# Performance work log

Hardware: AMD Instinct MI355X
Metric: run time of the kernel (lower is better)

The kernel has to match this reference:

```python
import jax, jax.numpy as jnp
import numpy as np

NEG = -9e15

def setup_inputs() -> dict:
    key = jax.random.key(0)
    k1, k2, k3, k4, k5, k6 = jax.random.split(key, 6)
    N, Fin, Fout = 8192, 256, 128
    inp = jax.random.normal(k1, (N, Fin), dtype=jnp.float32)
    adj = jax.random.randint(k2, (N, N), 0, 2, dtype=jnp.int32)
    W_w = jax.random.normal(k3, (Fout, Fin), dtype=jnp.float32) / np.sqrt(Fin)
    W_b = jax.random.normal(k4, (Fout,), dtype=jnp.float32) * 0.01
    a_w = jax.random.normal(k5, (1, 2 * Fout), dtype=jnp.float32) / np.sqrt(2 * Fout)
    a_b = jax.random.normal(k6, (1,), dtype=jnp.float32) * 0.01
    return {"input": inp, "adj": adj, "W_w": W_w, "W_b": W_b, "a_w": a_w, "a_b": a_b}

def reference(input, adj, W_w, W_b, a_w, a_b):
    alpha = 0.2
    Fout = W_w.shape[0]
    h = input @ W_w.T + W_b                      # [N, Fout]
    # a([h_i || h_j]) = a1.h_i + a2.h_j + b  (exact decomposition of concat+linear)
    a1 = a_w[0, :Fout]
    a2 = a_w[0, Fout:]
    e = jax.nn.leaky_relu((h @ a1)[:, None] + (h @ a2)[None, :] + a_b[0],
                          negative_slope=alpha)   # [N, N]
    scores = jnp.where(adj > 0, e, NEG)
    attention = jax.nn.softmax(scores, axis=1)    # dropout in eval mode = identity
    h_prime = attention @ h                       # [N, Fout]
    return jax.nn.elu(h_prime)
```

## Files before the change

kernel.cpp:

```cpp
#include <hip/hip_runtime.h>
#include <hip/hip_bf16.h>
#include <cmath>

#define NN 8192
#define FIN 256
#define FOUT 128
#define NCH 8
#define JC (NN / NCH)
#define WPC (JC / 64)
#define LOG2E 1.44269504f

typedef short short8 __attribute__((ext_vector_type(8)));
typedef float f32x4 __attribute__((ext_vector_type(4)));
typedef float f32x16 __attribute__((ext_vector_type(16)));
typedef unsigned long long u64;

static __device__ __forceinline__ unsigned short f2bf(float f) {
    unsigned u = __float_as_uint(f);
    u += 0x7fffu + ((u >> 16) & 1u);
    return (unsigned short)(u >> 16);
}

static __device__ __forceinline__ unsigned cvtpk(float lo, float hi) {
    unsigned r;
    asm("v_cvt_pk_bf16_f32 %0, %1, %2" : "=v"(r) : "v"(lo), "v"(hi));
    return r;
}

__global__ __launch_bounds__(256, 2)
void gat_stage(const float* __restrict__ input, const int* __restrict__ adj,
               const float* __restrict__ W, const float* __restrict__ Wb,
               const float* __restrict__ aw, const float* __restrict__ ab,
               unsigned short* __restrict__ hT4, float* __restrict__ s_out,
               float* __restrict__ t_out, u64* __restrict__ bm3) {
    __shared__ float sred[4][32];
    __shared__ float tred[4][32];
    const int tid = threadIdx.x;

    if (blockIdx.x >= 128) {
        const int row = (blockIdx.x - 128) * 2 + (tid >> 7);
        const int wing = tid & 127;
        const int4* p = (const int4*)(adj + (size_t)row * NN + wing * 64);
        u64 m = 0;
        #pragma unroll
        for (int q = 0; q < 16; ++q) {
            const int4 v = p[q];
            m |= (u64)(v.x > 0) << (q * 4 + 0);
            m |= (u64)(v.y > 0) << (q * 4 + 1);
            m |= (u64)(v.z > 0) << (q * 4 + 2);
            m |= (u64)(v.w > 0) << (q * 4 + 3);
        }
        const int ch = wing >> 4, winc = wing & 15;
        bm3[((size_t)ch * NN + row) * 16 + winc] = m;
        return;
    }

    const int w = tid >> 6, l = tid & 63;
    const int l5 = l >> 5, l31 = l & 31;
    const int nt = w >> 1, mh = w & 1;
    const int bx = blockIdx.x;
    const int i = bx * 64 + nt * 32 + l31;

    f32x16 acc0 = {}; f32x16 acc1 = {};
    #pragma unroll
    for (int ks = 0; ks < FIN / 16; ++ks) {
        const int c0 = ks * 16 + l5 * 8;
        const float4 b0 = *(const float4*)(input + (size_t)i * FIN + c0);
        const float4 b1 = *(const float4*)(input + (size_t)i * FIN + c0 + 4);
        short8 bf;
        bf[0]=(short)f2bf(b0.x); bf[1]=(short)f2bf(b0.y); bf[2]=(short)f2bf(b0.z); bf[3]=(short)f2bf(b0.w);
        bf[4]=(short)f2bf(b1.x); bf[5]=(short)f2bf(b1.y); bf[6]=(short)f2bf(b1.z); bf[7]=(short)f2bf(b1.w);
        {
            const int kcol = l31 + 32 * (2 * mh + 0);
            const float4 a0 = *(const float4*)(W + (size_t)kcol * FIN + c0);
            const float4 a1 = *(const float4*)(W + (size_t)kcol * FIN + c0 + 4);
            short8 af;
            af[0]=(short)f2bf(a0.x); af[1]=(short)f2bf(a0.y); af[2]=(short)f2bf(a0.z); af[3]=(short)f2bf(a0.w);
            af[4]=(short)f2bf(a1.x); af[5]=(short)f2bf(a1.y); af[6]=(short)f2bf(a1.z); af[7]=(short)f2bf(a1.w);
            acc0 = __builtin_amdgcn_mfma_f32_32x32x16_bf16(af, bf, acc0, 0, 0, 0);
        }
        {
            const int kcol = l31 + 32 * (2 * mh + 1);
            const float4 a0 = *(const float4*)(W + (size_t)kcol * FIN + c0);
            const float4 a1 = *(const float4*)(W + (size_t)kcol * FIN + c0 + 4);
            short8 af;
            af[0]=(short)f2bf(a0.x); af[1]=(short)f2bf(a0.y); af[2]=(short)f2bf(a0.z); af[3]=(short)f2bf(a0.w);
            af[4]=(short)f2bf(a1.x); af[5]=(short)f2bf(a1.y); af[6]=(short)f2bf(a1.z); af[7]=(short)f2bf(a1.w);
            acc1 = __builtin_amdgcn_mfma_f32_32x32x16_bf16(af, bf, acc1, 0, 0, 0);
        }
    }
    float sacc = 0.f, tacc = 0.f;
    const int jt = bx * 2 + nt;
    const int lane_half = 16 * (l31 >> 3);
    const int e4 = l31 & 7;
    #pragma unroll
    for (int m = 0; m < 2; ++m) {
        #pragma unroll
        for (int r = 0; r < 16; ++r) {
            const int kcol = 32 * (2 * mh + m) + 4 * l5 + (r & 3) + 8 * (r >> 2);
            const float hv = (m ? acc1[r] : acc0[r]) + Wb[kcol];
            const int lane4 = (kcol & 15) + lane_half;
            hT4[(size_t)(jt * 8 + (kcol >> 4)) * 512 + lane4 * 8 + e4] = f2bf(hv);
            sacc += hv * aw[kcol];
            tacc += hv * aw[FOUT + kcol];
        }
    }
    sacc += __shfl_xor(sacc, 32);
    tacc += __shfl_xor(tacc, 32);
    if (l < 32) { sred[w][l] = sacc; tred[w][l] = tacc; }
    __syncthreads();
    if (mh == 0 && l < 32) {
        s_out[i] = (sred[w][l] + sred[w + 1][l]) * LOG2E;
        t_out[i] = (tred[w][l] + tred[w + 1][l] + ab[0]) * LOG2E;
    }
}

__global__ __launch_bounds__(256, 4)
void gat_pass_b(const u64* __restrict__ bm3, const unsigned short* __restrict__ hT4,
                const float* __restrict__ s_in, const float* __restrict__ t_in,
                float* __restrict__ numw, float* __restrict__ dpart) {
    __shared__ int4 hbuf[2][1024];
    __shared__ float tlds[JC];
    const int tid = threadIdx.x;
    const int wv = tid >> 6, l = tid & 63;
    const int li = l & 15;
    const int kq = l >> 4;
    const int i0 = blockIdx.x * 64;
    const int chunk = blockIdx.y;
    const int jb = chunk * JC;

    *(float4*)&tlds[tid * 4] = *(const float4*)(t_in + jb + tid * 4);

    const int4* gsrc = (const int4*)hT4 + (size_t)chunk * 32 * 512;
    hbuf[0][tid]       = gsrc[tid];
    hbuf[0][tid + 256] = gsrc[tid + 256];
    hbuf[0][tid + 512] = gsrc[tid + 512];
    hbuf[0][tid + 768] = gsrc[tid + 768];

    const int lrow = wv * 16 + li;
    const float si = s_in[i0 + lrow];
    const u64* bmrow = bm3 + ((size_t)chunk * NN + i0 + lrow) * 16;
    u64 mcur = bmrow[0];
    __syncthreads();

    f32x4 acc0 = {}, acc1 = {}, acc2 = {}, acc3 = {};
    f32x4 acc4 = {}, acc5 = {}, acc6 = {}, acc7 = {};
    f32x4 accd = {};
    short8 ones;
    #pragma unroll
    for (int e = 0; e < 8; ++e) ones[e] = (short)0x3F80;

    for (int w = 0; w < WPC; ++w) {
        const int buf = w & 1;
        int4 g0, g1, g2, g3;
        u64 mnext = mcur;
        if (w + 1 < WPC) {
            const int4* gn = gsrc + (size_t)(w + 1) * 1024;
            g0 = gn[tid];
            g1 = gn[tid + 256];
            g2 = gn[tid + 512];
            g3 = gn[tid + 768];
            mnext = bmrow[w + 1];
        }
        #pragma unroll
        for (int kk = 0; kk < 2; ++kk) {
            const int4* hb = &hbuf[buf][kk * 512];
            const short8 af0 = *(const short8*)&hb[0 * 64 + l];
            const short8 af1 = *(const short8*)&hb[1 * 64 + l];
            const short8 af2 = *(const short8*)&hb[2 * 64 + l];
            const short8 af3 = *(const short8*)&hb[3 * 64 + l];
            const short8 af4 = *(const short8*)&hb[4 * 64 + l];
            const short8 af5 = *(const short8*)&hb[5 * 64 + l];
            const short8 af6 = *(const short8*)&hb[6 * 64 + l];
            const short8 af7 = *(const short8*)&hb[7 * 64 + l];
            const int tix = w * 64 + kk * 32 + kq * 8;
            const float4 t0 = *(const float4*)&tlds[tix];
            const float4 t1 = *(const float4*)&tlds[tix + 4];
            const unsigned mk = (unsigned)(mcur >> (kk * 32 + kq * 8)) & 0xffu;

            float x, p0, p1, p2, p3, p4, p5, p6, p7;
            x = si + t0.x; x = fmaxf(x, 0.2f * x); p0 = exp2f(x);
            p0 = (mk & 1u)   ? p0 : 0.f;
            x = si + t0.y; x = fmaxf(x, 0.2f * x); p1 = exp2f(x);
            p1 = (mk & 2u)   ? p1 : 0.f;
            x = si + t0.z; x = fmaxf(x, 0.2f * x); p2 = exp2f(x);
            p2 = (mk & 4u)   ? p2 : 0.f;
            x = si + t0.w; x = fmaxf(x, 0.2f * x); p3 = exp2f(x);
            p3 = (mk & 8u)   ? p3 : 0.f;
            x = si + t1.x; x = fmaxf(x, 0.2f * x); p4 = exp2f(x);
            p4 = (mk & 16u)  ? p4 : 0.f;
            x = si + t1.y; x = fmaxf(x, 0.2f * x); p5 = exp2f(x);
            p5 = (mk & 32u)  ? p5 : 0.f;
            x = si + t1.z; x = fmaxf(x, 0.2f * x); p6 = exp2f(x);
            p6 = (mk & 64u)  ? p6 : 0.f;
            x = si + t1.w; x = fmaxf(x, 0.2f * x); p7 = exp2f(x);
            p7 = (mk & 128u) ? p7 : 0.f;

            union { int4 i4; short8 s8; } bu;
            bu.i4.x = (int)cvtpk(p0, p1);
            bu.i4.y = (int)cvtpk(p2, p3);
            bu.i4.z = (int)cvtpk(p4, p5);
            bu.i4.w = (int)cvtpk(p6, p7);
            const short8 bf = bu.s8;

            acc0 = __builtin_amdgcn_mfma_f32_16x16x32_bf16(af0, bf, acc0, 0, 0, 0);
            acc1 = __builtin_amdgcn_mfma_f32_16x16x32_bf16(af1, bf, acc1, 0, 0, 0);
            acc2 = __builtin_amdgcn_mfma_f32_16x16x32_bf16(af2, bf, acc2, 0, 0, 0);
            acc3 = __builtin_amdgcn_mfma_f32_16x16x32_bf16(af3, bf, acc3, 0, 0, 0);
            acc4 = __builtin_amdgcn_mfma_f32_16x16x32_bf16(af4, bf, acc4, 0, 0, 0);
            acc5 = __builtin_amdgcn_mfma_f32_16x16x32_bf16(af5, bf, acc5, 0, 0, 0);
            acc6 = __builtin_amdgcn_mfma_f32_16x16x32_bf16(af6, bf, acc6, 0, 0, 0);
            acc7 = __builtin_amdgcn_mfma_f32_16x16x32_bf16(af7, bf, acc7, 0, 0, 0);
            accd = __builtin_amdgcn_mfma_f32_16x16x32_bf16(ones, bf, accd, 0, 0, 0);
        }
        if (w + 1 < WPC) {
            hbuf[buf ^ 1][tid]       = g0;
            hbuf[buf ^ 1][tid + 256] = g1;
            hbuf[buf ^ 1][tid + 512] = g2;
            hbuf[buf ^ 1][tid + 768] = g3;
        }
        mcur = mnext;
        __syncthreads();
    }

    float* nb = numw + (size_t)chunk * FOUT * NN;
    const int irow = i0 + lrow;
    #pragma unroll
    for (int r = 0; r < 4; ++r) {
        const int fr = kq * 4 + r;
        nb[(size_t)(fr      ) * NN + irow] = acc0[r];
        nb[(size_t)(fr + 16 ) * NN + irow] = acc1[r];
        nb[(size_t)(fr + 32 ) * NN + irow] = acc2[r];
        nb[(size_t)(fr + 48 ) * NN + irow] = acc3[r];
        nb[(size_t)(fr + 64 ) * NN + irow] = acc4[r];
        nb[(size_t)(fr + 80 ) * NN + irow] = acc5[r];
        nb[(size_t)(fr + 96 ) * NN + irow] = acc6[r];
        nb[(size_t)(fr + 112) * NN + irow] = acc7[r];
    }
    if (l < 16) dpart[(size_t)chunk * NN + i0 + wv * 16 + l] = accd[0];
}

__global__ __launch_bounds__(256)
void gat_reduce(const float* __restrict__ numw, const float* __restrict__ dpart,
                float* __restrict__ out, int nchunk) {
    __shared__ float tile[FOUT * 33];
    __shared__ float dent[32];
    const int t = threadIdx.x;
    const int i0 = blockIdx.x * 32;
    if (t < 32) {
        float d = 0.f;
        for (int c = 0; c < nchunk; ++c) d += dpart[(size_t)c * NN + i0 + t];
        dent[t] = d;
    }
    __syncthreads();
    #pragma unroll
    for (int e = 0; e < 4; ++e) {
        const int f = e * 32 + (t >> 3);
        const int io = (t & 7) * 4;
        float4 s = {0.f, 0.f, 0.f, 0.f};
        for (int c = 0; c < nchunk; ++c) {
            const float4 v = *(const float4*)(numw + ((size_t)c * FOUT + f) * NN + i0 + io);
            s.x += v.x; s.y += v.y; s.z += v.z; s.w += v.w;
        }
        float v;
        v = s.x / dent[io + 0]; tile[f * 33 + io + 0] = (v > 0.f) ? v : expm1f(v);
        v = s.y / dent[io + 1]; tile[f * 33 + io + 1] = (v > 0.f) ? v : expm1f(v);
        v = s.z / dent[io + 2]; tile[f * 33 + io + 2] = (v > 0.f) ? v : expm1f(v);
        v = s.w / dent[io + 3]; tile[f * 33 + io + 3] = (v > 0.f) ? v : expm1f(v);
    }
    __syncthreads();
    #pragma unroll
    for (int e = 0; e < 4; ++e) {
        const int row = (t >> 5) * 4 + e;
        const int fo = (t & 31) * 4;
        const float4 v = { tile[(fo + 0) * 33 + row], tile[(fo + 1) * 33 + row],
                           tile[(fo + 2) * 33 + row], tile[(fo + 3) * 33 + row] };
        *(float4*)(out + (size_t)(i0 + row) * FOUT + fo) = v;
    }
}

extern "C" void kernel_launch(void* const* d_in, const int* in_sizes, int n_in,
                              void* d_out, int out_size, void* d_ws, size_t ws_size,
                              hipStream_t stream) {
    const float* input = (const float*)d_in[0];
    const int*   adj   = (const int*)d_in[1];
    const float* Ww    = (const float*)d_in[2];
    const float* Wb    = (const float*)d_in[3];
    const float* aw    = (const float*)d_in[4];
    const float* ab    = (const float*)d_in[5];
    float* out = (float*)d_out;

    char* ws = (char*)d_ws;
    unsigned short* hT4 = (unsigned short*)ws;
    float* s_buf = (float*)(ws + (size_t)FOUT * NN * 2);
    float* t_buf = s_buf + NN;
    float* dpart = t_buf + NN;
    float* numw = dpart + (size_t)NCH * NN;
    u64* bm3 = (u64*)(numw + (size_t)NCH * NN * FOUT);

    gat_stage<<<dim3(128 + NN / 2), 256, 0, stream>>>(input, adj, Ww, Wb, aw, ab,
                                                      hT4, s_buf, t_buf, bm3);
    gat_pass_b<<<dim3(NN / 64, NCH), 256, 0, stream>>>(bm3, hT4, s_buf, t_buf, numw, dpart);
    gat_reduce<<<dim3(NN / 32), 256, 0, stream>>>(numw, dpart, out, NCH);
}
```

Baseline: 124.3 us.

## Process two row tiles per wave in pass B, reusing h fragments

Each block of pass B now covers 128 rows instead of 64, with each wave computing two 16-row tiles. Both tiles share the same LDS-loaded h fragments, so each fragment load feeds twice as many MFMAs and the h-chunk traffic from global memory is halved. The adjacency bitmask rows for the block are staged into padded LDS once, replacing the per-iteration global mask loads. In exchange, accumulator register pressure doubles (launch bounds drop from 4 to 2 blocks per SM) and the grid is half as large, which reduces occupancy and latency hiding.

```diff
diff --git a/kernel.cpp b/kernel.cpp
--- a/kernel.cpp
+++ b/kernel.cpp
@@ -8,6 +8,7 @@
 #define NCH 8
 #define JC (NN / NCH)
 #define WPC (JC / 64)
+#define MP 17
 #define LOG2E 1.44269504f
 
 typedef short short8 __attribute__((ext_vector_type(8)));
@@ -115,37 +116,73 @@
     }
 }
 
-__global__ __launch_bounds__(256, 4)
+#define PBUILD(SI, MK, BF)                                                      \
+    {                                                                           \
+        float x, p0, p1, p2, p3, p4, p5, p6, p7;                                \
+        x = (SI) + t0.x; x = fmaxf(x, 0.2f * x); p0 = exp2f(x);                 \
+        p0 = ((MK) & 1u)   ? p0 : 0.f;                                          \
+        x = (SI) + t0.y; x = fmaxf(x, 0.2f * x); p1 = exp2f(x);                 \
+        p1 = ((MK) & 2u)   ? p1 : 0.f;                                          \
+        x = (SI) + t0.z; x = fmaxf(x, 0.2f * x); p2 = exp2f(x);                 \
+        p2 = ((MK) & 4u)   ? p2 : 0.f;                                          \
+        x = (SI) + t0.w; x = fmaxf(x, 0.2f * x); p3 = exp2f(x);                 \
+        p3 = ((MK) & 8u)   ? p3 : 0.f;                                          \
+        x = (SI) + t1.x; x = fmaxf(x, 0.2f * x); p4 = exp2f(x);                 \
+        p4 = ((MK) & 16u)  ? p4 : 0.f;                                          \
+        x = (SI) + t1.y; x = fmaxf(x, 0.2f * x); p5 = exp2f(x);                 \
+        p5 = ((MK) & 32u)  ? p5 : 0.f;                                          \
+        x = (SI) + t1.z; x = fmaxf(x, 0.2f * x); p6 = exp2f(x);                 \
+        p6 = ((MK) & 64u)  ? p6 : 0.f;                                          \
+        x = (SI) + t1.w; x = fmaxf(x, 0.2f * x); p7 = exp2f(x);                 \
+        p7 = ((MK) & 128u) ? p7 : 0.f;                                          \
+        union { int4 i4; short8 s8; } bu;                                       \
+        bu.i4.x = (int)cvtpk(p0, p1);                                           \
+        bu.i4.y = (int)cvtpk(p2, p3);                                           \
+        bu.i4.z = (int)cvtpk(p4, p5);                                           \
+        bu.i4.w = (int)cvtpk(p6, p7);                                           \
+        BF = bu.s8;                                                             \
+    }
+
+__global__ __launch_bounds__(256, 2)
 void gat_pass_b(const u64* __restrict__ bm3, const unsigned short* __restrict__ hT4,
                 const float* __restrict__ s_in, const float* __restrict__ t_in,
                 float* __restrict__ numw, float* __restrict__ dpart) {
     __shared__ int4 hbuf[2][1024];
     __shared__ float tlds[JC];
+    __shared__ u64 mlds[128 * MP];
     const int tid = threadIdx.x;
     const int wv = tid >> 6, l = tid & 63;
     const int li = l & 15;
     const int kq = l >> 4;
-    const int i0 = blockIdx.x * 64;
+    const int i0 = blockIdx.x * 128;
     const int chunk = blockIdx.y;
-    const int jb = chunk * JC;
-
-    *(float4*)&tlds[tid * 4] = *(const float4*)(t_in + jb + tid * 4);
-
+    const int iw = i0 + wv * 32;
+
+    *(float4*)&tlds[tid * 4] = *(const float4*)(t_in + chunk * JC + tid * 4);
+    {
+        const uint4* src = (const uint4*)(bm3 + ((size_t)chunk * NN + i0) * 16) + tid * 4;
+        const uint4 q0 = src[0], q1 = src[1], q2 = src[2], q3 = src[3];
+        u64* dst = mlds + (tid >> 1) * MP + (tid & 1) * 8;
+        *(uint4*)(dst)     = q0;
+        *(uint4*)(dst + 2) = q1;
+        *(uint4*)(dst + 4) = q2;
+        *(uint4*)(dst + 6) = q3;
+    }
     const int4* gsrc = (const int4*)hT4 + (size_t)chunk * 32 * 512;
     hbuf[0][tid]       = gsrc[tid];
     hbuf[0][tid + 256] = gsrc[tid + 256];
     hbuf[0][tid + 512] = gsrc[tid + 512];
     hbuf[0][tid + 768] = gsrc[tid + 768];
 
-    const int lrow = wv * 16 + li;
-    const float si = s_in[i0 + lrow];
-    const u64* bmrow = bm3 + ((size_t)chunk * NN + i0 + lrow) * 16;
-    u64 mcur = bmrow[0];
+    const float si0 = s_in[iw + li];
+    const float si1 = s_in[iw + 16 + li];
+    const int mrow0 = (wv * 32 + li) * MP;
+    const int mrow1 = (wv * 32 + 16 + li) * MP;
     __syncthreads();
 
-    f32x4 acc0 = {}, acc1 = {}, acc2 = {}, acc3 = {};
-    f32x4 acc4 = {}, acc5 = {}, acc6 = {}, acc7 = {};
-    f32x4 accd = {};
+    f32x4 a00 = {}, a01 = {}, a02 = {}, a03 = {}, a04 = {}, a05 = {}, a06 = {}, a07 = {};
+    f32x4 a10 = {}, a11 = {}, a12 = {}, a13 = {}, a14 = {}, a15 = {}, a16 = {}, a17 = {};
+    f32x4 d0 = {}, d1 = {};
     short8 ones;
     #pragma unroll
     for (int e = 0; e < 8; ++e) ones[e] = (short)0x3F80;
@@ -153,15 +190,15 @@
     for (int w = 0; w < WPC; ++w) {
         const int buf = w & 1;
         int4 g0, g1, g2, g3;
-        u64 mnext = mcur;
         if (w + 1 < WPC) {
             const int4* gn = gsrc + (size_t)(w + 1) * 1024;
             g0 = gn[tid];
             g1 = gn[tid + 256];
             g2 = gn[tid + 512];
             g3 = gn[tid + 768];
-            mnext = bmrow[w + 1];
-        }
+        }
+        const u64 m0 = mlds[mrow0 + w];
+        const u64 m1 = mlds[mrow1 + w];
         #pragma unroll
         for (int kk = 0; kk < 2; ++kk) {
             const int4* hb = &hbuf[buf][kk * 512];
@@ -176,42 +213,31 @@
             const int tix = w * 64 + kk * 32 + kq * 8;
             const float4 t0 = *(const float4*)&tlds[tix];
             const float4 t1 = *(const float4*)&tlds[tix + 4];
-            const unsigned mk = (unsigned)(mcur >> (kk * 32 + kq * 8)) & 0xffu;
-
-            float x, p0, p1, p2, p3, p4, p5, p6, p7;
-            x = si + t0.x; x = fmaxf(x, 0.2f * x); p0 = exp2f(x);
-            p0 = (mk & 1u)   ? p0 : 0.f;
-            x = si + t0.y; x = fmaxf(x, 0.2f * x); p1 = exp2f(x);
-            p1 = (mk & 2u)   ? p1 : 0.f;
-            x = si + t0.z; x = fmaxf(x, 0.2f * x); p2 = exp2f(x);
-            p2 = (mk & 4u)   ? p2 : 0.f;
-            x = si + t0.w; x = fmaxf(x, 0.2f * x); p3 = exp2f(x);
-            p3 = (mk & 8u)   ? p3 : 0.f;
-            x = si + t1.x; x = fmaxf(x, 0.2f * x); p4 = exp2f(x);
-            p4 = (mk & 16u)  ? p4 : 0.f;
-            x = si + t1.y; x = fmaxf(x, 0.2f * x); p5 = exp2f(x);
-            p5 = (mk & 32u)  ? p5 : 0.f;
-            x = si + t1.z; x = fmaxf(x, 0.2f * x); p6 = exp2f(x);
-            p6 = (mk & 64u)  ? p6 : 0.f;
-            x = si + t1.w; x = fmaxf(x, 0.2f * x); p7 = exp2f(x);
-            p7 = (mk & 128u) ? p7 : 0.f;
-
-            union { int4 i4; short8 s8; } bu;
-            bu.i4.x = (int)cvtpk(p0, p1);
-            bu.i4.y = (int)cvtpk(p2, p3);
-            bu.i4.z = (int)cvtpk(p4, p5);
-            bu.i4.w = (int)cvtpk(p6, p7);
-            const short8 bf = bu.s8;
-
-            acc0 = __builtin_amdgcn_mfma_f32_16x16x32_bf16(af0, bf, acc0, 0, 0, 0);
-            acc1 = __builtin_amdgcn_mfma_f32_16x16x32_bf16(af1, bf, acc1, 0, 0, 0);
-            acc2 = __builtin_amdgcn_mfma_f32_16x16x32_bf16(af2, bf, acc2, 0, 0, 0);
-            acc3 = __builtin_amdgcn_mfma_f32_16x16x32_bf16(af3, bf, acc3, 0, 0, 0);
-            acc4 = __builtin_amdgcn_mfma_f32_16x16x32_bf16(af4, bf, acc4, 0, 0, 0);
-            acc5 = __builtin_amdgcn_mfma_f32_16x16x32_bf16(af5, bf, acc5, 0, 0, 0);
-            acc6 = __builtin_amdgcn_mfma_f32_16x16x32_bf16(af6, bf, acc6, 0, 0, 0);
-            acc7 = __builtin_amdgcn_mfma_f32_16x16x32_bf16(af7, bf, acc7, 0, 0, 0);
-            accd = __builtin_amdgcn_mfma_f32_16x16x32_bf16(ones, bf, accd, 0, 0, 0);
+            const unsigned mk0 = (unsigned)(m0 >> (kk * 32 + kq * 8)) & 0xffu;
+            const unsigned mk1 = (unsigned)(m1 >> (kk * 32 + kq * 8)) & 0xffu;
+
+            short8 bf0, bf1;
+            PBUILD(si0, mk0, bf0)
+            PBUILD(si1, mk1, bf1)
+
+            a00 = __builtin_amdgcn_mfma_f32_16x16x32_bf16(af0, bf0, a00, 0, 0, 0);
+            a01 = __builtin_amdgcn_mfma_f32_16x16x32_bf16(af1, bf0, a01, 0, 0, 0);
+            a02 = __builtin_amdgcn_mfma_f32_16x16x32_bf16(af2, bf0, a02, 0, 0, 0);
+            a03 = __builtin_amdgcn_mfma_f32_16x16x32_bf16(af3, bf0, a03, 0, 0, 0);
+            a04 = __builtin_amdgcn_mfma_f32_16x16x32_bf16(af4, bf0, a04, 0, 0, 0);
+            a05 = __builtin_amdgcn_mfma_f32_16x16x32_bf16(af5, bf0, a05, 0, 0, 0);
+            a06 = __builtin_amdgcn_mfma_f32_16x16x32_bf16(af6, bf0, a06, 0, 0, 0);
+            a07 = __builtin_amdgcn_mfma_f32_16x16x32_bf16(af7, bf0, a07, 0, 0, 0);
+            d0  = __builtin_amdgcn_mfma_f32_16x16x32_bf16(ones, bf0, d0, 0, 0, 0);
+            a10 = __builtin_amdgcn_mfma_f32_16x16x32_bf16(af0, bf1, a10, 0, 0, 0);
+            a11 = __builtin_amdgcn_mfma_f32_16x16x32_bf16(af1, bf1, a11, 0, 0, 0);
+            a12 = __builtin_amdgcn_mfma_f32_16x16x32_bf16(af2, bf1, a12, 0, 0, 0);
+            a13 = __builtin_amdgcn_mfma_f32_16x16x32_bf16(af3, bf1, a13, 0, 0, 0);
+            a14 = __builtin_amdgcn_mfma_f32_16x16x32_bf16(af4, bf1, a14, 0, 0, 0);
+            a15 = __builtin_amdgcn_mfma_f32_16x16x32_bf16(af5, bf1, a15, 0, 0, 0);
+            a16 = __builtin_amdgcn_mfma_f32_16x16x32_bf16(af6, bf1, a16, 0, 0, 0);
+            a17 = __builtin_amdgcn_mfma_f32_16x16x32_bf16(af7, bf1, a17, 0, 0, 0);
+            d1  = __builtin_amdgcn_mfma_f32_16x16x32_bf16(ones, bf1, d1, 0, 0, 0);
         }
         if (w + 1 < WPC) {
             hbuf[buf ^ 1][tid]       = g0;
@@ -219,25 +245,36 @@
             hbuf[buf ^ 1][tid + 512] = g2;
             hbuf[buf ^ 1][tid + 768] = g3;
         }
-        mcur = mnext;
         __syncthreads();
     }
 
     float* nb = numw + (size_t)chunk * FOUT * NN;
-    const int irow = i0 + lrow;
+    const int ir0 = iw + li;
+    const int ir1 = iw + 16 + li;
     #pragma unroll
     for (int r = 0; r < 4; ++r) {
         const int fr = kq * 4 + r;
-        nb[(size_t)(fr      ) * NN + irow] = acc0[r];
-        nb[(size_t)(fr + 16 ) * NN + irow] = acc1[r];
-        nb[(size_t)(fr + 32 ) * NN + irow] = acc2[r];
-        nb[(size_t)(fr + 48 ) * NN + irow] = acc3[r];
-        nb[(size_t)(fr + 64 ) * NN + irow] = acc4[r];
-        nb[(size_t)(fr + 80 ) * NN + irow] = acc5[r];
-        nb[(size_t)(fr + 96 ) * NN + irow] = acc6[r];
-        nb[(size_t)(fr + 112) * NN + irow] = acc7[r];
-    }
-    if (l < 16) dpart[(size_t)chunk * NN + i0 + wv * 16 + l] = accd[0];
+        nb[(size_t)(fr      ) * NN + ir0] = a00[r];
+        nb[(size_t)(fr + 16 ) * NN + ir0] = a01[r];
+        nb[(size_t)(fr + 32 ) * NN + ir0] = a02[r];
+        nb[(size_t)(fr + 48 ) * NN + ir0] = a03[r];
+        nb[(size_t)(fr + 64 ) * NN + ir0] = a04[r];
+        nb[(size_t)(fr + 80 ) * NN + ir0] = a05[r];
+        nb[(size_t)(fr + 96 ) * NN + ir0] = a06[r];
+        nb[(size_t)(fr + 112) * NN + ir0] = a07[r];
+        nb[(size_t)(fr      ) * NN + ir1] = a10[r];
+        nb[(size_t)(fr + 16 ) * NN + ir1] = a11[r];
+        nb[(size_t)(fr + 32 ) * NN + ir1] = a12[r];
+        nb[(size_t)(fr + 48 ) * NN + ir1] = a13[r];
+        nb[(size_t)(fr + 64 ) * NN + ir1] = a14[r];
+        nb[(size_t)(fr + 80 ) * NN + ir1] = a15[r];
+        nb[(size_t)(fr + 96 ) * NN + ir1] = a16[r];
+        nb[(size_t)(fr + 112) * NN + ir1] = a17[r];
+    }
+    if (kq == 0) {
+        dpart[(size_t)chunk * NN + ir0] = d0[0];
+        dpart[(size_t)chunk * NN + ir1] = d1[0];
+    }
 }
 
 __global__ __launch_bounds__(256)
@@ -300,6 +337,6 @@
 
     gat_stage<<<dim3(128 + NN / 2), 256, 0, stream>>>(input, adj, Ww, Wb, aw, ab,
                                                       hT4, s_buf, t_buf, bm3);
-    gat_pass_b<<<dim3(NN / 64, NCH), 256, 0, stream>>>(bm3, hT4, s_buf, t_buf, numw, dpart);
+    gat_pass_b<<<dim3(NN / 128, NCH), 256, 0, stream>>>(bm3, hT4, s_buf, t_buf, numw, dpart);
     gat_reduce<<<dim3(NN / 32), 256, 0, stream>>>(numw, dpart, out, NCH);
 }
```

Measured after the change: 127.5 us. +2.6%, slower.
